# Kernel optimization log

Measured on AMD Instinct MI355X. Metric: run time of the kernel, lower is better.

Reference implementation:

```python
import jax, jax.numpy as jnp
import numpy as np

SCALE = 1.0  # std of the Normal error model (init arg `scale`)
B, P, D, T = 32, 256, 64, 4096


def setup_inputs() -> dict:
    key = jax.random.key(0)
    k1, k2, k3 = jax.random.split(key, 3)
    data = jax.random.normal(k1, (B, P, D), dtype=jnp.float32)
    targets = jax.random.normal(k2, (B, P), dtype=jnp.float32)
    task_pool = jax.random.normal(k3, (T, D, 1), dtype=jnp.float32)
    return {"data": data, "targets": targets, "task_pool": task_pool}


def reference(data, targets, task_pool):
    # W: (n_dims, n_tasks), matching task_pool.squeeze(-1).T in the original
    W = task_pool[..., 0].T
    dt = data.dtype

    # Per-point, per-task predictions and Gaussian log-likelihoods, computed ONCE.
    # The original recomputes X@W and the log-prob sum for every prefix i (O(n^2));
    # here a single cumsum over the point axis reproduces the same prefix sums.
    pred_per_task = jnp.einsum('bpd,dt->bpt', data, W)          # (B, P, T)
    err = targets[..., None] - pred_per_task                     # (B, P, T)
    log_norm = -jnp.log(jnp.asarray(SCALE, dt)) - 0.5 * jnp.log(jnp.asarray(2.0 * np.pi, dt))
    scores = -0.5 * (err / SCALE) ** 2 + log_norm                # Normal(0, scale).log_prob

    cum = jnp.cumsum(scores, axis=1)                             # cum[:, i] = sum_{j<=i}
    # Posterior for predicting point i uses points 0..i-1; point 0 uses a uniform
    # posterior (original: W.mean(dim=1) == softmax(zeros) @ W.T).
    log_lik = jnp.concatenate([jnp.zeros_like(cum[:, :1]), cum[:, :-1]], axis=1)
    post = jax.nn.softmax(log_lik, axis=-1)                      # (B, P, T)

    w_mmse = jnp.einsum('bpt,dt->bpd', post, W)                  # posterior-mean weights
    return jnp.einsum('bpd,bpd->bp', data, w_mmse)               # (B, P)
```

## Files before the change

kernel.cpp:

```cpp
#include <hip/hip_runtime.h>
#include <hip/hip_bf16.h>
#include <math.h>

#define Bb 32
#define Pp 256
#define Dd 64
#define Tt 4096

typedef unsigned short ushort_t;
typedef __attribute__((ext_vector_type(8))) short bf16x8;
typedef __attribute__((ext_vector_type(4))) float f32x4;

#define TRIP2_BYTES ((size_t)Bb * Pp * 128 * 16)
#define TRIP_BYTES  ((size_t)Bb * Pp * 64 * 16)

__device__ __forceinline__ void split8(const float* __restrict__ x,
                                       bf16x8& hi, bf16x8& lo) {
#pragma unroll
  for (int j = 0; j < 8; ++j) {
    const __hip_bfloat16 hb = __float2bfloat16(x[j]);
    const float hf = __bfloat162float(hb);
    const __hip_bfloat16 lb = __float2bfloat16(x[j] - hf);
    hi[j] = *(const short*)&hb;
    lo[j] = *(const short*)&lb;
  }
}

#define MFMA6(a)                                                     \
  a = __builtin_amdgcn_mfma_f32_16x16x32_bf16(ah0, bh0, a, 0, 0, 0); \
  a = __builtin_amdgcn_mfma_f32_16x16x32_bf16(ah1, bh1, a, 0, 0, 0); \
  a = __builtin_amdgcn_mfma_f32_16x16x32_bf16(ah0, bl0, a, 0, 0, 0); \
  a = __builtin_amdgcn_mfma_f32_16x16x32_bf16(al0, bh0, a, 0, 0, 0); \
  a = __builtin_amdgcn_mfma_f32_16x16x32_bf16(ah1, bl1, a, 0, 0, 0); \
  a = __builtin_amdgcn_mfma_f32_16x16x32_bf16(al1, bh1, a, 0, 0, 0);

__global__ __launch_bounds__(256, 4) void k_main2(const float* __restrict__ data,
                                                  const float* __restrict__ Wt,
                                                  const float* __restrict__ targets,
                                                  float4* __restrict__ triples) {
  __shared__ short Bhs[128 * 72];
  __shared__ short Bls[128 * 72];
  const int tid  = threadIdx.x;
  const int wid  = tid >> 6;
  const int lane = tid & 63;
  const int quad = lane >> 4;
  const int l16  = lane & 15;
  const int b     = blockIdx.x >> 5;
  const int strip = blockIdx.x & 31;
  const int t0    = strip * 128;

  {
    const float4* src = (const float4*)(Wt + (size_t)t0 * Dd);
#pragma unroll
    for (int j = 0; j < 8; ++j) {
      const int idx = tid + j * 256;
      const int tl  = idx >> 4;
      const int col = (idx & 15) * 4;
      const float4 v = src[idx];
      const float xs[4] = {v.x, v.y, v.z, v.w};
      short h4[4], l4[4];
#pragma unroll
      for (int u = 0; u < 4; ++u) {
        const __hip_bfloat16 hb = __float2bfloat16(xs[u]);
        const float hf = __bfloat162float(hb);
        const __hip_bfloat16 lb = __float2bfloat16(xs[u] - hf);
        h4[u] = *(const short*)&hb;
        l4[u] = *(const short*)&lb;
      }
      *(short4*)&Bhs[tl * 72 + col] = make_short4(h4[0], h4[1], h4[2], h4[3]);
      *(short4*)&Bls[tl * 72 + col] = make_short4(l4[0], l4[1], l4[2], l4[3]);
    }
  }
  __syncthreads();

  const float* __restrict__ abase = data + (size_t)b * Pp * Dd;
  float4* __restrict__ trb = triples + (size_t)b * Pp * 128;
  const int wstrip = strip * 4 + wid;

  float R[2];
  R[0] = 0.f; R[1] = 0.f;

#pragma unroll 1
  for (int sg = 0; sg < 16; ++sg) {
    const int p0 = sg * 16;
    bf16x8 ah0, al0, ah1, al1;
    {
      const float* ar = abase + (size_t)(p0 + l16) * Dd;
      float a0[8], a1[8];
      *(float4*)&a0[0] = *(const float4*)(ar + quad * 8);
      *(float4*)&a0[4] = *(const float4*)(ar + quad * 8 + 4);
      *(float4*)&a1[0] = *(const float4*)(ar + 32 + quad * 8);
      *(float4*)&a1[4] = *(const float4*)(ar + 32 + quad * 8 + 4);
      split8(a0, ah0, al0);
      split8(a1, ah1, al1);
    }
    const float4 tq = *(const float4*)(targets + b * Pp + p0 + quad * 4);

    float cc[2][4], av[2][4];
#pragma unroll
    for (int nt = 0; nt < 2; ++nt) {
      const int tl = wid * 32 + nt * 16 + l16;
      const int bo = tl * 72 + quad * 8;
      const bf16x8 bh0 = *(const bf16x8*)&Bhs[bo];
      const bf16x8 bh1 = *(const bf16x8*)&Bhs[bo + 32];
      const bf16x8 bl0 = *(const bf16x8*)&Bls[bo];
      const bf16x8 bl1 = *(const bf16x8*)&Bls[bo + 32];
      f32x4 a = (f32x4)0.f;
      MFMA6(a)

      float sc[4];
      { const float e = tq.x - a[0]; sc[0] = -0.5f * e * e; }
      { const float e = tq.y - a[1]; sc[1] = -0.5f * e * e; }
      { const float e = tq.z - a[2]; sc[2] = -0.5f * e * e; }
      { const float e = tq.w - a[3]; sc[3] = -0.5f * e * e; }

      const float colsum = (sc[0] + sc[1]) + (sc[2] + sc[3]);
      const float x1 = __shfl_xor(colsum, 16, 64);
      const float x2 = __shfl_xor(colsum, 32, 64);
      const float x3 = __shfl_xor(x1, 32, 64);
      const float pre = (quad == 0) ? 0.f
                      : (quad == 1) ? x1
                      : (quad == 2) ? (x2 + x3)
                                    : (x1 + x2 + x3);
      const float base = R[nt] + pre;
      cc[nt][0] = base;
      cc[nt][1] = base + sc[0];
      cc[nt][2] = cc[nt][1] + sc[1];
      cc[nt][3] = cc[nt][2] + sc[2];
#pragma unroll
      for (int r = 0; r < 4; ++r) av[nt][r] = a[r];

      R[nt] += ((colsum + x1) + (x2 + x3));
    }

    float mm[4], ss[4], vv[4];
#pragma unroll
    for (int r = 0; r < 4; ++r) {
      mm[r] = fmaxf(cc[0][r], cc[1][r]);
      const float e0 = __expf(cc[0][r] - mm[r]);
      const float e1 = __expf(cc[1][r] - mm[r]);
      ss[r] = e0 + e1;
      vv[r] = fmaf(e0, av[0][r], e1 * av[1][r]);
    }

    float M[4];
#pragma unroll
    for (int r = 0; r < 4; ++r) M[r] = mm[r];
#pragma unroll
    for (int off = 1; off < 16; off <<= 1)
#pragma unroll
      for (int r = 0; r < 4; ++r) M[r] = fmaxf(M[r], __shfl_xor(M[r], off, 64));
#pragma unroll
    for (int r = 0; r < 4; ++r) {
      const float f = __expf(mm[r] - M[r]);
      ss[r] *= f; vv[r] *= f;
    }
#pragma unroll
    for (int off = 1; off < 16; off <<= 1)
#pragma unroll
      for (int r = 0; r < 4; ++r) {
        ss[r] += __shfl_xor(ss[r], off, 64);
        vv[r] += __shfl_xor(vv[r], off, 64);
      }

    if (l16 == 0) {
#pragma unroll
      for (int r = 0; r < 4; ++r) {
        const int p = p0 + quad * 4 + r;
        trb[p * 128 + wstrip] = make_float4(M[r], ss[r], vv[r], 0.f);
      }
    }
  }
}

__global__ __launch_bounds__(256) void k_merge2(const float4* __restrict__ ws,
                                                float* __restrict__ out) {
  const int gt   = blockIdx.x * 256 + threadIdx.x;
  const int bp   = gt >> 6;
  const int lane = gt & 63;
  const float4 o0 = ws[(size_t)bp * 128 + lane];
  const float4 o1 = ws[(size_t)bp * 128 + 64 + lane];
  float M = fmaxf(o0.x, o1.x);
  const float g0 = __expf(o0.x - M), g1 = __expf(o1.x - M);
  float S = g0 * o0.y + g1 * o1.y;
  float V = g0 * o0.z + g1 * o1.z;
#pragma unroll
  for (int off = 1; off < 64; off <<= 1) {
    const float mo = __shfl_xor(M, off, 64);
    const float so = __shfl_xor(S, off, 64);
    const float vo = __shfl_xor(V, off, 64);
    const float mn = fmaxf(M, mo);
    const float f0 = __expf(M - mn), f1 = __expf(mo - mn);
    S = S * f0 + so * f1;
    V = V * f0 + vo * f1;
    M = mn;
  }
  if (lane == 0) out[bp] = V / S;
}

__global__ __launch_bounds__(256) void k_scan_fused(const float* __restrict__ data,
                                                    const float* __restrict__ targets,
                                                    const float* __restrict__ task_pool,
                                                    float4* __restrict__ ws) {
  const int b     = blockIdx.x >> 4;
  const int wid   = threadIdx.x >> 6;
  const int lane  = threadIdx.x & 63;
  const int chunk = ((blockIdx.x & 15) << 2) | wid;
  const int t     = (chunk << 6) | lane;
  float w[Dd];
#pragma unroll
  for (int d = 0; d < Dd; d += 4) {
    const float4 r = *(const float4*)(task_pool + (size_t)t * Dd + d);
    w[d] = r.x; w[d + 1] = r.y; w[d + 2] = r.z; w[d + 3] = r.w;
  }
  const float* drow = data + (size_t)b * (Pp * Dd);
  const float* tgt  = targets + b * Pp;
  float4* wsb       = ws + (size_t)b * (Pp * 64);
  float c = 0.f;
  for (int p = 0; p < Pp; ++p) {
    float a0 = 0.f, a1 = 0.f, a2 = 0.f, a3 = 0.f;
    const float* r = drow + p * Dd;
#pragma unroll
    for (int d = 0; d < Dd; d += 4) {
      a0 = fmaf(r[d], w[d], a0);         a1 = fmaf(r[d + 1], w[d + 1], a1);
      a2 = fmaf(r[d + 2], w[d + 2], a2); a3 = fmaf(r[d + 3], w[d + 3], a3);
    }
    const float pred = (a0 + a1) + (a2 + a3);
    float m = c;
#pragma unroll
    for (int off = 32; off; off >>= 1) m = fmaxf(m, __shfl_xor(m, off, 64));
    const float e = __expf(c - m);
    float s = e, v = e * pred;
#pragma unroll
    for (int off = 32; off; off >>= 1) {
      s += __shfl_xor(s, off, 64);
      v += __shfl_xor(v, off, 64);
    }
    if (lane == 0) wsb[p * 64 + chunk] = make_float4(m, s, v, 0.f);
    const float err = tgt[p] - pred;
    c = fmaf(-0.5f * err, err, c);
  }
}

__global__ __launch_bounds__(256) void k_merge(const float4* __restrict__ ws,
                                               float* __restrict__ out) {
  const int gt   = blockIdx.x * 256 + threadIdx.x;
  const int bp   = gt >> 6;
  const int lane = gt & 63;
  const float4 o = ws[(size_t)bp * 64 + lane];
  const float m = o.x, s = o.y, v = o.z;
  float M = m;
#pragma unroll
  for (int off = 32; off; off >>= 1) M = fmaxf(M, __shfl_xor(M, off, 64));
  const float f = __expf(m - M);
  float S = f * s, V = f * v;
#pragma unroll
  for (int off = 32; off; off >>= 1) {
    S += __shfl_xor(S, off, 64);
    V += __shfl_xor(V, off, 64);
  }
  if (lane == 0) out[bp] = V / S;
}

extern "C" void kernel_launch(void* const* d_in, const int* in_sizes, int n_in,
                              void* d_out, int out_size, void* d_ws, size_t ws_size,
                              hipStream_t stream) {
  const float* data      = (const float*)d_in[0];
  const float* targets   = (const float*)d_in[1];
  const float* task_pool = (const float*)d_in[2];
  float* out = (float*)d_out;

  if (ws_size >= TRIP2_BYTES) {
    float4* trips = (float4*)d_ws;
    k_main2<<<dim3(Bb * 32), dim3(256), 0, stream>>>(data, task_pool, targets, trips);
    k_merge2<<<dim3((Bb * Pp * 64) / 256), dim3(256), 0, stream>>>(trips, out);
  } else {
    float4* triples = (float4*)d_ws;
    k_scan_fused<<<dim3(512), dim3(256), 0, stream>>>(data, targets, task_pool, triples);
    k_merge<<<dim3((Bb * Pp * 64) / 256), dim3(256), 0, stream>>>(triples, out);
  }
}
```

Baseline: 113.8 us.

## Precompute bf16 hi/lo splits in a separate kernel and use DPP row reductions

Adds a conversion kernel that splits data and task_pool into bf16 hi/lo arrays in the workspace once per call. Previously each of the 32 strip blocks per batch redid this split for the same data rows. The main kernel now loads pre-split fragments straight from global memory, keeps the B fragments in registers instead of LDS, and drops the shared-memory staging and its barrier. The 16-lane max and sum reductions switch from shfl_xor to DPP row rotates. The cost is an extra launch, extra workspace, and the global write and re-read of the converted arrays.

```diff
diff --git a/kernel.cpp b/kernel.cpp
--- a/kernel.cpp
+++ b/kernel.cpp
@@ -12,19 +12,9 @@
 typedef __attribute__((ext_vector_type(4))) float f32x4;
 
 #define TRIP2_BYTES ((size_t)Bb * Pp * 128 * 16)
-#define TRIP_BYTES  ((size_t)Bb * Pp * 64 * 16)
-
-__device__ __forceinline__ void split8(const float* __restrict__ x,
-                                       bf16x8& hi, bf16x8& lo) {
-#pragma unroll
-  for (int j = 0; j < 8; ++j) {
-    const __hip_bfloat16 hb = __float2bfloat16(x[j]);
-    const float hf = __bfloat162float(hb);
-    const __hip_bfloat16 lb = __float2bfloat16(x[j] - hf);
-    hi[j] = *(const short*)&hb;
-    lo[j] = *(const short*)&lb;
-  }
-}
+#define A_BF_BYTES  ((size_t)Bb * Pp * Dd * 2)
+#define B_BF_BYTES  ((size_t)Tt * Dd * 2)
+#define WS_NEED     (TRIP2_BYTES + 2 * A_BF_BYTES + 2 * B_BF_BYTES)
 
 #define MFMA6(a)                                                     \
   a = __builtin_amdgcn_mfma_f32_16x16x32_bf16(ah0, bh0, a, 0, 0, 0); \
@@ -34,12 +24,37 @@
   a = __builtin_amdgcn_mfma_f32_16x16x32_bf16(ah1, bl1, a, 0, 0, 0); \
   a = __builtin_amdgcn_mfma_f32_16x16x32_bf16(al1, bh1, a, 0, 0, 0);
 
-__global__ __launch_bounds__(256, 4) void k_main2(const float* __restrict__ data,
-                                                  const float* __restrict__ Wt,
+template <int CTRL>
+__device__ __forceinline__ float dpp_rot(float x) {
+  return __int_as_float(__builtin_amdgcn_update_dpp(
+      0, __float_as_int(x), CTRL, 0xF, 0xF, true));
+}
+#define ROW_ROR_8 0x128
+#define ROW_ROR_4 0x124
+#define ROW_ROR_2 0x122
+#define ROW_ROR_1 0x121
+
+__global__ __launch_bounds__(256) void k_conv(const float* __restrict__ data,
+                                              const float* __restrict__ Wt,
+                                              ushort_t* __restrict__ Ah, ushort_t* __restrict__ Al,
+                                              ushort_t* __restrict__ Bh, ushort_t* __restrict__ Bl) {
+  const int i  = blockIdx.x * 256 + threadIdx.x;
+  const int NA = Bb * Pp * Dd;
+  const float x = (i < NA) ? data[i] : Wt[i - NA];
+  const __hip_bfloat16 h = __float2bfloat16(x);
+  const float hf = __bfloat162float(h);
+  const __hip_bfloat16 l = __float2bfloat16(x - hf);
+  if (i < NA) { Ah[i] = *(const ushort_t*)&h; Al[i] = *(const ushort_t*)&l; }
+  else        { const int j = i - NA;
+                Bh[j] = *(const ushort_t*)&h; Bl[j] = *(const ushort_t*)&l; }
+}
+
+__global__ __launch_bounds__(256, 4) void k_main3(const ushort_t* __restrict__ Ah,
+                                                  const ushort_t* __restrict__ Al,
+                                                  const ushort_t* __restrict__ Bh,
+                                                  const ushort_t* __restrict__ Bl,
                                                   const float* __restrict__ targets,
                                                   float4* __restrict__ triples) {
-  __shared__ short Bhs[128 * 72];
-  __shared__ short Bls[128 * 72];
   const int tid  = threadIdx.x;
   const int wid  = tid >> 6;
   const int lane = tid & 63;
@@ -49,31 +64,18 @@
   const int strip = blockIdx.x & 31;
   const int t0    = strip * 128;
 
-  {
-    const float4* src = (const float4*)(Wt + (size_t)t0 * Dd);
-#pragma unroll
-    for (int j = 0; j < 8; ++j) {
-      const int idx = tid + j * 256;
-      const int tl  = idx >> 4;
-      const int col = (idx & 15) * 4;
-      const float4 v = src[idx];
-      const float xs[4] = {v.x, v.y, v.z, v.w};
-      short h4[4], l4[4];
-#pragma unroll
-      for (int u = 0; u < 4; ++u) {
-        const __hip_bfloat16 hb = __float2bfloat16(xs[u]);
-        const float hf = __bfloat162float(hb);
-        const __hip_bfloat16 lb = __float2bfloat16(xs[u] - hf);
-        h4[u] = *(const short*)&hb;
-        l4[u] = *(const short*)&lb;
-      }
-      *(short4*)&Bhs[tl * 72 + col] = make_short4(h4[0], h4[1], h4[2], h4[3]);
-      *(short4*)&Bls[tl * 72 + col] = make_short4(l4[0], l4[1], l4[2], l4[3]);
-    }
-  }
-  __syncthreads();
-
-  const float* __restrict__ abase = data + (size_t)b * Pp * Dd;
+  bf16x8 Bf[2][4];
+#pragma unroll
+  for (int nt = 0; nt < 2; ++nt) {
+    const size_t brow = (size_t)(t0 + wid * 32 + nt * 16 + l16) * Dd + quad * 8;
+    Bf[nt][0] = *(const bf16x8*)(Bh + brow);
+    Bf[nt][1] = *(const bf16x8*)(Bh + brow + 32);
+    Bf[nt][2] = *(const bf16x8*)(Bl + brow);
+    Bf[nt][3] = *(const bf16x8*)(Bl + brow + 32);
+  }
+
+  const ushort_t* __restrict__ ahb = Ah + (size_t)b * Pp * Dd;
+  const ushort_t* __restrict__ alb = Al + (size_t)b * Pp * Dd;
   float4* __restrict__ trb = triples + (size_t)b * Pp * 128;
   const int wstrip = strip * 4 + wid;
 
@@ -83,28 +85,18 @@
 #pragma unroll 1
   for (int sg = 0; sg < 16; ++sg) {
     const int p0 = sg * 16;
-    bf16x8 ah0, al0, ah1, al1;
-    {
-      const float* ar = abase + (size_t)(p0 + l16) * Dd;
-      float a0[8], a1[8];
-      *(float4*)&a0[0] = *(const float4*)(ar + quad * 8);
-      *(float4*)&a0[4] = *(const float4*)(ar + quad * 8 + 4);
-      *(float4*)&a1[0] = *(const float4*)(ar + 32 + quad * 8);
-      *(float4*)&a1[4] = *(const float4*)(ar + 32 + quad * 8 + 4);
-      split8(a0, ah0, al0);
-      split8(a1, ah1, al1);
-    }
+    const size_t aoff = (size_t)(p0 + l16) * Dd + quad * 8;
+    const bf16x8 ah0 = *(const bf16x8*)(ahb + aoff);
+    const bf16x8 ah1 = *(const bf16x8*)(ahb + aoff + 32);
+    const bf16x8 al0 = *(const bf16x8*)(alb + aoff);
+    const bf16x8 al1 = *(const bf16x8*)(alb + aoff + 32);
     const float4 tq = *(const float4*)(targets + b * Pp + p0 + quad * 4);
 
     float cc[2][4], av[2][4];
 #pragma unroll
     for (int nt = 0; nt < 2; ++nt) {
-      const int tl = wid * 32 + nt * 16 + l16;
-      const int bo = tl * 72 + quad * 8;
-      const bf16x8 bh0 = *(const bf16x8*)&Bhs[bo];
-      const bf16x8 bh1 = *(const bf16x8*)&Bhs[bo + 32];
-      const bf16x8 bl0 = *(const bf16x8*)&Bls[bo];
-      const bf16x8 bl1 = *(const bf16x8*)&Bls[bo + 32];
+      const bf16x8 bh0 = Bf[nt][0], bh1 = Bf[nt][1];
+      const bf16x8 bl0 = Bf[nt][2], bl1 = Bf[nt][3];
       f32x4 a = (f32x4)0.f;
       MFMA6(a)
 
@@ -145,23 +137,24 @@
 
     float M[4];
 #pragma unroll
-    for (int r = 0; r < 4; ++r) M[r] = mm[r];
-#pragma unroll
-    for (int off = 1; off < 16; off <<= 1)
-#pragma unroll
-      for (int r = 0; r < 4; ++r) M[r] = fmaxf(M[r], __shfl_xor(M[r], off, 64));
+    for (int r = 0; r < 4; ++r) {
+      float m = mm[r];
+      m = fmaxf(m, dpp_rot<ROW_ROR_8>(m));
+      m = fmaxf(m, dpp_rot<ROW_ROR_4>(m));
+      m = fmaxf(m, dpp_rot<ROW_ROR_2>(m));
+      m = fmaxf(m, dpp_rot<ROW_ROR_1>(m));
+      M[r] = m;
+    }
 #pragma unroll
     for (int r = 0; r < 4; ++r) {
       const float f = __expf(mm[r] - M[r]);
-      ss[r] *= f; vv[r] *= f;
-    }
-#pragma unroll
-    for (int off = 1; off < 16; off <<= 1)
-#pragma unroll
-      for (int r = 0; r < 4; ++r) {
-        ss[r] += __shfl_xor(ss[r], off, 64);
-        vv[r] += __shfl_xor(vv[r], off, 64);
-      }
+      float s = ss[r] * f, v = vv[r] * f;
+      s += dpp_rot<ROW_ROR_8>(s);  v += dpp_rot<ROW_ROR_8>(v);
+      s += dpp_rot<ROW_ROR_4>(s);  v += dpp_rot<ROW_ROR_4>(v);
+      s += dpp_rot<ROW_ROR_2>(s);  v += dpp_rot<ROW_ROR_2>(v);
+      s += dpp_rot<ROW_ROR_1>(s);  v += dpp_rot<ROW_ROR_1>(v);
+      ss[r] = s; vv[r] = v;
+    }
 
     if (l16 == 0) {
 #pragma unroll
@@ -270,9 +263,16 @@
   const float* task_pool = (const float*)d_in[2];
   float* out = (float*)d_out;
 
-  if (ws_size >= TRIP2_BYTES) {
-    float4* trips = (float4*)d_ws;
-    k_main2<<<dim3(Bb * 32), dim3(256), 0, stream>>>(data, task_pool, targets, trips);
+  if (ws_size >= WS_NEED) {
+    float4*   trips = (float4*)d_ws;
+    char*     cb    = (char*)d_ws + TRIP2_BYTES;
+    ushort_t* Ah    = (ushort_t*)cb;
+    ushort_t* Al    = (ushort_t*)(cb + A_BF_BYTES);
+    ushort_t* Bh    = (ushort_t*)(cb + 2 * A_BF_BYTES);
+    ushort_t* Bl    = (ushort_t*)(cb + 2 * A_BF_BYTES + B_BF_BYTES);
+    k_conv  <<<dim3((Bb * Pp * Dd + Tt * Dd) / 256), dim3(256), 0, stream>>>(
+        data, task_pool, Ah, Al, Bh, Bl);
+    k_main3 <<<dim3(Bb * 32), dim3(256), 0, stream>>>(Ah, Al, Bh, Bl, targets, trips);
     k_merge2<<<dim3((Bb * Pp * 64) / 256), dim3(256), 0, stream>>>(trips, out);
   } else {
     float4* triples = (float4*)d_ws;
```

After: 108.9 us. 4.3% less time.
